# Kernel optimization log

Hardware: AMD Instinct MI355X
Metric: run time of the kernel (lower is better)

Reference implementation:

```python
import jax, jax.numpy as jnp
import numpy as np

N = 50000      # nodes
E = 800000     # edges (avg degree 16)
D_IN = 64
D_OUT = 64


def setup_inputs() -> dict:
    key = jax.random.key(0)
    k1, k2, k3 = jax.random.split(key, 3)
    x = jax.random.normal(k1, (N, D_IN), dtype=jnp.float32)
    edge_index = jax.random.randint(k2, (2, E), 0, N, dtype=jnp.int32)
    W = jax.random.normal(k3, (D_OUT, D_IN), dtype=jnp.float32) * 0.05
    b = jnp.zeros((D_OUT,), dtype=jnp.float32)
    prelu_a = jnp.full((1,), 0.25, dtype=jnp.float32)  # nn.PReLU() default
    return {"x": x, "edge_index": edge_index, "W": W, "b": b, "prelu_a": prelu_a}


def reference(x, edge_index, W, b, prelu_a):
    # GCNConv (PyG, normalize=True, add_self_loops=True) + PReLU.
    # Dropout is identity at inference and omitted.
    n = x.shape[0]
    row, col = edge_index[0], edge_index[1]
    loop = jnp.arange(n, dtype=edge_index.dtype)
    row = jnp.concatenate([row, loop])  # [E+N] source nodes
    col = jnp.concatenate([col, loop])  # [E+N] target nodes

    # Symmetric degree normalization: deg over targets (edge weight = 1).
    ones = jnp.ones(row.shape[0], dtype=x.dtype)
    deg = jax.ops.segment_sum(ones, col, num_segments=n)          # [N]
    dinv = jnp.where(deg > 0, jax.lax.rsqrt(deg), 0.0)            # deg^{-1/2}
    norm = dinv[row] * dinv[col]                                  # [E+N]

    h = x @ W.T                                                   # [N, D_OUT]
    msg = h[row] * norm[:, None]                                  # gather + scale
    out = jax.ops.segment_sum(msg, col, num_segments=n) + b       # scatter-add

    # PReLU with a single shared slope parameter
    return jnp.where(out >= 0, out, prelu_a * out)
```

## Files before the change

kernel.cpp:

```cpp
#include <hip/hip_runtime.h>
#include <hip/hip_bf16.h>

#define D 64
#define CAP 64
#define GROUPS 8
#define ZERO_BLOCKS 49

typedef float f32x4 __attribute__((ext_vector_type(4)));

__device__ __forceinline__ float bflo(unsigned u) {
    union { unsigned i; float f; } x; x.i = u << 16; return x.f;
}
__device__ __forceinline__ float bfhi(unsigned u) {
    union { unsigned i; float f; } x; x.i = u & 0xffff0000u; return x.f;
}

__global__ void __launch_bounds__(256) gemm_zero_kernel(
    const float* __restrict__ x, const float* __restrict__ W,
    __hip_bfloat16* __restrict__ h, int4* __restrict__ cnt4, int nzero4, int n)
{
    if (blockIdx.x < ZERO_BLOCKS) {
        int i = blockIdx.x * 256 + threadIdx.x;
        if (i < nzero4) cnt4[i] = make_int4(0, 0, 0, 0);
    }

    __shared__ float Ws[D * 65];
    __shared__ float xs[4][D];

    int tid = threadIdx.x;
    #pragma unroll
    for (int k = 0; k < 16; ++k) {
        int idx = tid + k * 256;
        int o = idx >> 6, i = idx & 63;
        Ws[o * 65 + i] = W[idx];
    }

    int ln = tid >> 6;
    int o  = tid & 63;
    int node = blockIdx.x * 4 + ln;
    if (node < n) {
        xs[ln][o] = x[node * D + o];
    }
    __syncthreads();

    if (node >= n) return;

    float sum = 0.0f;
    #pragma unroll
    for (int i = 0; i < D; ++i) {
        sum += xs[ln][i] * Ws[o * 65 + i];
    }
    h[(size_t)node * D + o] = __float2bfloat16(sum);
}

__global__ void __launch_bounds__(256) fill_kernel(
    const int* __restrict__ row, const int* __restrict__ col,
    const int4* __restrict__ row4, const int4* __restrict__ col4,
    int* __restrict__ cnt, unsigned short* __restrict__ srcs,
    int* __restrict__ ovf_cnt, int2* __restrict__ ovf, int E, int E4, int n)
{
    int g   = blockIdx.x & (GROUPS - 1);
    int bg  = blockIdx.x >> 3;
    int bpg = gridDim.x >> 3;
    int npg = (n + GROUPS - 1) / GROUPS;
    int lo  = g * npg;
    int hi  = lo + npg < n ? lo + npg : n;
    int stride = bpg * 256;

    for (int i = bg * 256 + threadIdx.x; i < E4; i += stride) {
        int4 cc = col4[i];
        int4 rr = row4[i];
        #pragma unroll
        for (int j = 0; j < 4; ++j) {
            int c = (j == 0) ? cc.x : (j == 1) ? cc.y : (j == 2) ? cc.z : cc.w;
            int r = (j == 0) ? rr.x : (j == 1) ? rr.y : (j == 2) ? rr.z : rr.w;
            if (c >= lo && c < hi) {
                int slot = atomicAdd(&cnt[c], 1);
                if (slot < CAP) {
                    srcs[(size_t)c * CAP + slot] = (unsigned short)r;
                } else {
                    int oi = atomicAdd(ovf_cnt, 1);
                    ovf[oi] = make_int2(r, c);
                }
            }
        }
    }
    for (int e = E4 * 4 + bg * 256 + threadIdx.x; e < E; e += stride) {
        int c = col[e];
        if (c >= lo && c < hi) {
            int r = row[e];
            int slot = atomicAdd(&cnt[c], 1);
            if (slot < CAP) {
                srcs[(size_t)c * CAP + slot] = (unsigned short)r;
            } else {
                int oi = atomicAdd(ovf_cnt, 1);
                ovf[oi] = make_int2(r, c);
            }
        }
    }
}

__global__ void __launch_bounds__(256) gather_kernel(
    const int* __restrict__ cnt, const unsigned short* __restrict__ srcs,
    const __hip_bfloat16* __restrict__ h,
    const float* __restrict__ b, const float* __restrict__ prelu_a,
    const int* __restrict__ ovf_cnt, const int2* __restrict__ ovf,
    float* __restrict__ out, int n)
{
    int wave = (blockIdx.x * blockDim.x + threadIdx.x) >> 6;
    int lane = threadIdx.x & 63;
    if (wave >= n) return;
    int c = wave;
    int g = lane >> 3;
    int q = lane & 7;

    int deg = cnt[c];
    int m = deg < CAP ? deg : CAP;
    float dc = rsqrtf((float)deg + 1.0f);

    int   s  = 0;
    float wl = 0.0f;
    if (lane < m) {
        s  = (int)__builtin_nontemporal_load(&srcs[(size_t)c * CAP + lane]);
        wl = rsqrtf((float)cnt[s] + 1.0f) * dc;
    }

    float acc[8] = {0.f, 0.f, 0.f, 0.f, 0.f, 0.f, 0.f, 0.f};

    int m8 = (m + 7) & ~7;
    for (int k = 0; k < m8; k += 8) {
        int   sk = __shfl(s,  k + g);
        float wk = __shfl(wl, k + g);
        uint4 v = *reinterpret_cast<const uint4*>(&h[(size_t)sk * D + q * 8]);
        acc[0] += wk * bflo(v.x);  acc[1] += wk * bfhi(v.x);
        acc[2] += wk * bflo(v.y);  acc[3] += wk * bfhi(v.y);
        acc[4] += wk * bflo(v.z);  acc[5] += wk * bfhi(v.z);
        acc[6] += wk * bflo(v.w);  acc[7] += wk * bfhi(v.w);
    }

    #pragma unroll
    for (int j = 0; j < 8; ++j) {
        acc[j] += __shfl_xor(acc[j], 8);
        acc[j] += __shfl_xor(acc[j], 16);
        acc[j] += __shfl_xor(acc[j], 32);
    }

    if (g == 0) {
        uint4 hv = *reinterpret_cast<const uint4*>(&h[(size_t)c * D + q * 8]);
        float dc2 = dc * dc;
        float hc[8] = { bflo(hv.x), bfhi(hv.x), bflo(hv.y), bfhi(hv.y),
                        bflo(hv.z), bfhi(hv.z), bflo(hv.w), bfhi(hv.w) };
        #pragma unroll
        for (int j = 0; j < 8; ++j) {
            acc[j] += hc[j] * dc2 + b[q * 8 + j];
        }

        int nov = *ovf_cnt;
        for (int i = 0; i < nov; ++i) {
            int2 rc = ovf[i];
            if (rc.y == c) {
                float wo = rsqrtf((float)cnt[rc.x] + 1.0f) * dc;
                uint4 ov = *reinterpret_cast<const uint4*>(&h[(size_t)rc.x * D + q * 8]);
                float of[8] = { bflo(ov.x), bfhi(ov.x), bflo(ov.y), bfhi(ov.y),
                                bflo(ov.z), bfhi(ov.z), bflo(ov.w), bfhi(ov.w) };
                #pragma unroll
                for (int j = 0; j < 8; ++j) acc[j] += of[j] * wo;
            }
        }

        float al = prelu_a[0];
        #pragma unroll
        for (int j = 0; j < 8; ++j) {
            acc[j] = acc[j] >= 0.0f ? acc[j] : al * acc[j];
        }
        f32x4 o0 = { acc[0], acc[1], acc[2], acc[3] };
        f32x4 o1 = { acc[4], acc[5], acc[6], acc[7] };
        f32x4* op = (f32x4*)&out[(size_t)c * D + q * 8];
        __builtin_nontemporal_store(o0, op);
        __builtin_nontemporal_store(o1, op + 1);
    }
}

extern "C" void kernel_launch(void* const* d_in, const int* in_sizes, int n_in,
                              void* d_out, int out_size, void* d_ws, size_t ws_size,
                              hipStream_t stream) {
    const float* x       = (const float*)d_in[0];
    const int*   eidx    = (const int*)d_in[1];
    const float* W       = (const float*)d_in[2];
    const float* b       = (const float*)d_in[3];
    const float* prelu_a = (const float*)d_in[4];

    const int E = in_sizes[1] / 2;
    const int n = in_sizes[0] / D;
    const int* row = eidx;
    const int* col = eidx + E;

    float* out = (float*)d_out;

    int E4 = 0;
    if ((E % 4) == 0 &&
        ((uintptr_t)row % 16) == 0 && ((uintptr_t)col % 16) == 0) {
        E4 = E / 4;
    }

    __hip_bfloat16* h    = (__hip_bfloat16*)d_ws;
    unsigned short* srcs = (unsigned short*)(h + (size_t)n * D);
    int*   cnt     = (int*)(srcs + (size_t)n * CAP);
    int*   ovf_cnt = cnt + n;
    int2*  ovf     = (int2*)(cnt + n + 2);

    int nzero4 = (n + 1 + 3) / 4;

    gemm_zero_kernel<<<(n + 3) / 4, 256, 0, stream>>>(
        x, W, h, (int4*)cnt, nzero4, n);

    fill_kernel<<<2048, 256, 0, stream>>>(
        row, col, (const int4*)row, (const int4*)col,
        cnt, srcs, ovf_cnt, ovf, E, E4, n);

    gather_kernel<<<(n * 64 + 255) / 256, 256, 0, stream>>>(
        cnt, srcs, h, b, prelu_a, ovf_cnt, ovf, out, n);
}
```

Baseline: 101.7 us.

## Fuse GEMM, CSR fill and gather into one cooperative persistent kernel

Merges the three launches into a single cooperative kernel: the counter zeroing and the GEMM, then the bucketed edge fill, then the gather. Phases are separated by grid-wide syncs, and all loops are grid-strided over a grid sized from occupancy. The gather phase now gives each block group a node range matching its fill group, so waves loop over destination nodes. The aim is to remove inter-kernel launch gaps and tail effects. In exchange it adds grid barriers, fewer concurrently scheduled blocks for the GEMM, and an occupancy query on the host.

```diff
diff --git a/kernel.cpp b/kernel.cpp
--- a/kernel.cpp
+++ b/kernel.cpp
@@ -1,10 +1,12 @@
 #include <hip/hip_runtime.h>
 #include <hip/hip_bf16.h>
+#include <hip/hip_cooperative_groups.h>
+
+namespace cg = cooperative_groups;
 
 #define D 64
 #define CAP 64
-#define GROUPS 8
-#define ZERO_BLOCKS 49
+#define NGRP 8
 
 typedef float f32x4 __attribute__((ext_vector_type(4)));
 
@@ -15,66 +17,81 @@
     union { unsigned i; float f; } x; x.i = u & 0xffff0000u; return x.f;
 }
 
-__global__ void __launch_bounds__(256) gemm_zero_kernel(
+__global__ void __launch_bounds__(256, 8) mega_kernel(
     const float* __restrict__ x, const float* __restrict__ W,
-    __hip_bfloat16* __restrict__ h, int4* __restrict__ cnt4, int nzero4, int n)
+    const float* __restrict__ b, const float* __restrict__ prelu_a,
+    const int* __restrict__ row, const int* __restrict__ col,
+    const int4* __restrict__ row4, const int4* __restrict__ col4,
+    int E, int E4, int n,
+    __hip_bfloat16* __restrict__ h, unsigned short* __restrict__ srcs,
+    int* __restrict__ cnt, int* __restrict__ ovf_cnt, int2* __restrict__ ovf,
+    float* __restrict__ out)
 {
-    if (blockIdx.x < ZERO_BLOCKS) {
-        int i = blockIdx.x * 256 + threadIdx.x;
-        if (i < nzero4) cnt4[i] = make_int4(0, 0, 0, 0);
+    cg::grid_group grid = cg::this_grid();
+    const int tid = threadIdx.x;
+    const int nb  = gridDim.x;
+
+    {
+        int nzero4 = (n + 2 + 3) >> 2;
+        int gt = blockIdx.x * 256 + tid;
+        if (gt < nzero4) ((int4*)cnt)[gt] = make_int4(0, 0, 0, 0);
     }
 
     __shared__ float Ws[D * 65];
     __shared__ float xs[4][D];
-
-    int tid = threadIdx.x;
     #pragma unroll
     for (int k = 0; k < 16; ++k) {
         int idx = tid + k * 256;
-        int o = idx >> 6, i = idx & 63;
-        Ws[o * 65 + i] = W[idx];
-    }
-
-    int ln = tid >> 6;
-    int o  = tid & 63;
-    int node = blockIdx.x * 4 + ln;
-    if (node < n) {
-        xs[ln][o] = x[node * D + o];
-    }
-    __syncthreads();
-
-    if (node >= n) return;
-
-    float sum = 0.0f;
-    #pragma unroll
-    for (int i = 0; i < D; ++i) {
-        sum += xs[ln][i] * Ws[o * 65 + i];
-    }
-    h[(size_t)node * D + o] = __float2bfloat16(sum);
-}
-
-__global__ void __launch_bounds__(256) fill_kernel(
-    const int* __restrict__ row, const int* __restrict__ col,
-    const int4* __restrict__ row4, const int4* __restrict__ col4,
-    int* __restrict__ cnt, unsigned short* __restrict__ srcs,
-    int* __restrict__ ovf_cnt, int2* __restrict__ ovf, int E, int E4, int n)
-{
-    int g   = blockIdx.x & (GROUPS - 1);
-    int bg  = blockIdx.x >> 3;
-    int bpg = gridDim.x >> 3;
-    int npg = (n + GROUPS - 1) / GROUPS;
-    int lo  = g * npg;
-    int hi  = lo + npg < n ? lo + npg : n;
-    int stride = bpg * 256;
-
-    for (int i = bg * 256 + threadIdx.x; i < E4; i += stride) {
-        int4 cc = col4[i];
-        int4 rr = row4[i];
-        #pragma unroll
-        for (int j = 0; j < 4; ++j) {
-            int c = (j == 0) ? cc.x : (j == 1) ? cc.y : (j == 2) ? cc.z : cc.w;
-            int r = (j == 0) ? rr.x : (j == 1) ? rr.y : (j == 2) ? rr.z : rr.w;
+        Ws[(idx >> 6) * 65 + (idx & 63)] = W[idx];
+    }
+    const int ln = tid >> 6, o = tid & 63;
+    const int nquad = (n + 3) >> 2;
+    for (int q = blockIdx.x; q < nquad; q += nb) {
+        int node = q * 4 + ln;
+        __syncthreads();
+        if (node < n) xs[ln][o] = x[(size_t)node * D + o];
+        __syncthreads();
+        if (node < n) {
+            float sum = 0.0f;
+            #pragma unroll
+            for (int i = 0; i < D; ++i) sum += xs[ln][i] * Ws[o * 65 + i];
+            h[(size_t)node * D + o] = __float2bfloat16(sum);
+        }
+    }
+
+    grid.sync();
+
+    {
+        int g   = blockIdx.x & (NGRP - 1);
+        int bg  = blockIdx.x >> 3;
+        int bpg = nb >> 3;
+        int npg = (n + NGRP - 1) / NGRP;
+        int lo  = g * npg;
+        int hi  = lo + npg < n ? lo + npg : n;
+        int stride = bpg * 256;
+
+        for (int i = bg * 256 + tid; i < E4; i += stride) {
+            int4 cc = col4[i];
+            int4 rr = row4[i];
+            #pragma unroll
+            for (int j = 0; j < 4; ++j) {
+                int c = (j == 0) ? cc.x : (j == 1) ? cc.y : (j == 2) ? cc.z : cc.w;
+                int r = (j == 0) ? rr.x : (j == 1) ? rr.y : (j == 2) ? rr.z : rr.w;
+                if (c >= lo && c < hi) {
+                    int slot = atomicAdd(&cnt[c], 1);
+                    if (slot < CAP) {
+                        srcs[(size_t)c * CAP + slot] = (unsigned short)r;
+                    } else {
+                        int oi = atomicAdd(ovf_cnt, 1);
+                        ovf[oi] = make_int2(r, c);
+                    }
+                }
+            }
+        }
+        for (int e = E4 * 4 + bg * 256 + tid; e < E; e += stride) {
+            int c = col[e];
             if (c >= lo && c < hi) {
+                int r = row[e];
                 int slot = atomicAdd(&cnt[c], 1);
                 if (slot < CAP) {
                     srcs[(size_t)c * CAP + slot] = (unsigned short)r;
@@ -85,99 +102,87 @@
             }
         }
     }
-    for (int e = E4 * 4 + bg * 256 + threadIdx.x; e < E; e += stride) {
-        int c = col[e];
-        if (c >= lo && c < hi) {
-            int r = row[e];
-            int slot = atomicAdd(&cnt[c], 1);
-            if (slot < CAP) {
-                srcs[(size_t)c * CAP + slot] = (unsigned short)r;
-            } else {
-                int oi = atomicAdd(ovf_cnt, 1);
-                ovf[oi] = make_int2(r, c);
-            }
-        }
-    }
-}
-
-__global__ void __launch_bounds__(256) gather_kernel(
-    const int* __restrict__ cnt, const unsigned short* __restrict__ srcs,
-    const __hip_bfloat16* __restrict__ h,
-    const float* __restrict__ b, const float* __restrict__ prelu_a,
-    const int* __restrict__ ovf_cnt, const int2* __restrict__ ovf,
-    float* __restrict__ out, int n)
-{
-    int wave = (blockIdx.x * blockDim.x + threadIdx.x) >> 6;
-    int lane = threadIdx.x & 63;
-    if (wave >= n) return;
-    int c = wave;
-    int g = lane >> 3;
-    int q = lane & 7;
-
-    int deg = cnt[c];
-    int m = deg < CAP ? deg : CAP;
-    float dc = rsqrtf((float)deg + 1.0f);
-
-    int   s  = 0;
-    float wl = 0.0f;
-    if (lane < m) {
-        s  = (int)__builtin_nontemporal_load(&srcs[(size_t)c * CAP + lane]);
-        wl = rsqrtf((float)cnt[s] + 1.0f) * dc;
-    }
-
-    float acc[8] = {0.f, 0.f, 0.f, 0.f, 0.f, 0.f, 0.f, 0.f};
-
-    int m8 = (m + 7) & ~7;
-    for (int k = 0; k < m8; k += 8) {
-        int   sk = __shfl(s,  k + g);
-        float wk = __shfl(wl, k + g);
-        uint4 v = *reinterpret_cast<const uint4*>(&h[(size_t)sk * D + q * 8]);
-        acc[0] += wk * bflo(v.x);  acc[1] += wk * bfhi(v.x);
-        acc[2] += wk * bflo(v.y);  acc[3] += wk * bfhi(v.y);
-        acc[4] += wk * bflo(v.z);  acc[5] += wk * bfhi(v.z);
-        acc[6] += wk * bflo(v.w);  acc[7] += wk * bfhi(v.w);
-    }
-
-    #pragma unroll
-    for (int j = 0; j < 8; ++j) {
-        acc[j] += __shfl_xor(acc[j], 8);
-        acc[j] += __shfl_xor(acc[j], 16);
-        acc[j] += __shfl_xor(acc[j], 32);
-    }
-
-    if (g == 0) {
-        uint4 hv = *reinterpret_cast<const uint4*>(&h[(size_t)c * D + q * 8]);
-        float dc2 = dc * dc;
-        float hc[8] = { bflo(hv.x), bfhi(hv.x), bflo(hv.y), bfhi(hv.y),
-                        bflo(hv.z), bfhi(hv.z), bflo(hv.w), bfhi(hv.w) };
+
+    grid.sync();
+
+    {
+        int g   = blockIdx.x & (NGRP - 1);
+        int bg  = blockIdx.x >> 3;
+        int bpg = nb >> 3;
+        int npg = (n + NGRP - 1) / NGRP;
+        int lo  = g * npg;
+        int hi  = lo + npg < n ? lo + npg : n;
+        int lane = tid & 63;
+        int wig  = bg * 4 + (tid >> 6);
+        int wpg  = bpg * 4;
+        int gg   = lane >> 3;
+        int q    = lane & 7;
+
+        int nov = *ovf_cnt;
+        float al = prelu_a[0];
+        float bq[8];
         #pragma unroll
-        for (int j = 0; j < 8; ++j) {
-            acc[j] += hc[j] * dc2 + b[q * 8 + j];
-        }
-
-        int nov = *ovf_cnt;
-        for (int i = 0; i < nov; ++i) {
-            int2 rc = ovf[i];
-            if (rc.y == c) {
-                float wo = rsqrtf((float)cnt[rc.x] + 1.0f) * dc;
-                uint4 ov = *reinterpret_cast<const uint4*>(&h[(size_t)rc.x * D + q * 8]);
-                float of[8] = { bflo(ov.x), bfhi(ov.x), bflo(ov.y), bfhi(ov.y),
-                                bflo(ov.z), bfhi(ov.z), bflo(ov.w), bfhi(ov.w) };
+        for (int j = 0; j < 8; ++j) bq[j] = b[q * 8 + j];
+
+        for (int c = lo + wig; c < hi; c += wpg) {
+            int deg = cnt[c];
+            int m = deg < CAP ? deg : CAP;
+            float dc = rsqrtf((float)deg + 1.0f);
+
+            int   s  = 0;
+            float wl = 0.0f;
+            if (lane < m) {
+                s  = (int)srcs[(size_t)c * CAP + lane];
+                wl = rsqrtf((float)cnt[s] + 1.0f) * dc;
+            }
+
+            float acc[8] = {0.f, 0.f, 0.f, 0.f, 0.f, 0.f, 0.f, 0.f};
+            int m8 = (m + 7) & ~7;
+            for (int k = 0; k < m8; k += 8) {
+                int   sk = __shfl(s,  k + gg);
+                float wk = __shfl(wl, k + gg);
+                uint4 v = *reinterpret_cast<const uint4*>(&h[(size_t)sk * D + q * 8]);
+                acc[0] += wk * bflo(v.x);  acc[1] += wk * bfhi(v.x);
+                acc[2] += wk * bflo(v.y);  acc[3] += wk * bfhi(v.y);
+                acc[4] += wk * bflo(v.z);  acc[5] += wk * bfhi(v.z);
+                acc[6] += wk * bflo(v.w);  acc[7] += wk * bfhi(v.w);
+            }
+            #pragma unroll
+            for (int j = 0; j < 8; ++j) {
+                acc[j] += __shfl_xor(acc[j], 8);
+                acc[j] += __shfl_xor(acc[j], 16);
+                acc[j] += __shfl_xor(acc[j], 32);
+            }
+            if (gg == 0) {
+                uint4 hv = *reinterpret_cast<const uint4*>(&h[(size_t)c * D + q * 8]);
+                float dc2 = dc * dc;
+                float hc[8] = { bflo(hv.x), bfhi(hv.x), bflo(hv.y), bfhi(hv.y),
+                                bflo(hv.z), bfhi(hv.z), bflo(hv.w), bfhi(hv.w) };
                 #pragma unroll
-                for (int j = 0; j < 8; ++j) acc[j] += of[j] * wo;
-            }
-        }
-
-        float al = prelu_a[0];
-        #pragma unroll
-        for (int j = 0; j < 8; ++j) {
-            acc[j] = acc[j] >= 0.0f ? acc[j] : al * acc[j];
-        }
-        f32x4 o0 = { acc[0], acc[1], acc[2], acc[3] };
-        f32x4 o1 = { acc[4], acc[5], acc[6], acc[7] };
-        f32x4* op = (f32x4*)&out[(size_t)c * D + q * 8];
-        __builtin_nontemporal_store(o0, op);
-        __builtin_nontemporal_store(o1, op + 1);
+                for (int j = 0; j < 8; ++j) acc[j] += hc[j] * dc2 + bq[j];
+
+                for (int i = 0; i < nov; ++i) {
+                    int2 rc = ovf[i];
+                    if (rc.y == c) {
+                        float wo = rsqrtf((float)cnt[rc.x] + 1.0f) * dc;
+                        uint4 ov = *reinterpret_cast<const uint4*>(&h[(size_t)rc.x * D + q * 8]);
+                        acc[0] += wo * bflo(ov.x);  acc[1] += wo * bfhi(ov.x);
+                        acc[2] += wo * bflo(ov.y);  acc[3] += wo * bfhi(ov.y);
+                        acc[4] += wo * bflo(ov.z);  acc[5] += wo * bfhi(ov.z);
+                        acc[6] += wo * bflo(ov.w);  acc[7] += wo * bfhi(ov.w);
+                    }
+                }
+                #pragma unroll
+                for (int j = 0; j < 8; ++j) {
+                    acc[j] = acc[j] >= 0.0f ? acc[j] : al * acc[j];
+                }
+                f32x4 o0 = { acc[0], acc[1], acc[2], acc[3] };
+                f32x4 o1 = { acc[4], acc[5], acc[6], acc[7] };
+                f32x4* op = (f32x4*)&out[(size_t)c * D + q * 8];
+                __builtin_nontemporal_store(o0, op);
+                __builtin_nontemporal_store(o1, op + 1);
+            }
+        }
     }
 }
 
@@ -190,10 +195,12 @@
     const float* b       = (const float*)d_in[3];
     const float* prelu_a = (const float*)d_in[4];
 
-    const int E = in_sizes[1] / 2;
-    const int n = in_sizes[0] / D;
+    int E = in_sizes[1] / 2;
+    int n = in_sizes[0] / D;
     const int* row = eidx;
     const int* col = eidx + E;
+    const int4* row4 = (const int4*)row;
+    const int4* col4 = (const int4*)col;
 
     float* out = (float*)d_out;
 
@@ -209,15 +216,20 @@
     int*   ovf_cnt = cnt + n;
     int2*  ovf     = (int2*)(cnt + n + 2);
 
-    int nzero4 = (n + 1 + 3) / 4;
-
-    gemm_zero_kernel<<<(n + 3) / 4, 256, 0, stream>>>(
-        x, W, h, (int4*)cnt, nzero4, n);
-
-    fill_kernel<<<2048, 256, 0, stream>>>(
-        row, col, (const int4*)row, (const int4*)col,
-        cnt, srcs, ovf_cnt, ovf, E, E4, n);
-
-    gather_kernel<<<(n * 64 + 255) / 256, 256, 0, stream>>>(
-        cnt, srcs, h, b, prelu_a, ovf_cnt, ovf, out, n);
-}
+    int occ = 0;
+    hipOccupancyMaxActiveBlocksPerMultiprocessor(&occ, (const void*)mega_kernel, 256, 0);
+    int nb = occ * 256;
+    if (nb > 2048) nb = 2048;
+    nb &= ~7;
+    if (nb <= 0) nb = 512;
+
+    void* args[] = {
+        (void*)&x, (void*)&W, (void*)&b, (void*)&prelu_a,
+        (void*)&row, (void*)&col, (void*)&row4, (void*)&col4,
+        (void*)&E, (void*)&E4, (void*)&n,
+        (void*)&h, (void*)&srcs, (void*)&cnt, (void*)&ovf_cnt, (void*)&ovf,
+        (void*)&out
+    };
+    hipLaunchCooperativeKernel((const void*)mega_kernel,
+                               dim3(nb), dim3(256), args, 0, stream);
+}
```

Result: slower. 395.7 us (+289.0%).
